# Kernel tuning notes

Hardware: AMD Instinct MI355X
Metric: run time of the kernel (lower is better)

Reference implementation:

```python
import jax, jax.numpy as jnp
import numpy as np

N, E, D = 100000, 1600000, 128


def setup_inputs() -> dict:
    key = jax.random.key(0)
    ks = jax.random.split(key, 8)
    s = 1.0 / np.sqrt(D)
    return {
        "x": jax.random.normal(ks[0], (N, D), dtype=jnp.float32),
        "edge_index": jax.random.randint(ks[1], (2, E), 0, N, dtype=jnp.int64),
        "x_prev": jax.random.normal(ks[2], (N, D), dtype=jnp.float32),
        # GCNConv params: weight [in,out], bias [out]
        "W": jax.random.uniform(ks[3], (D, D), jnp.float32, -s, s),
        "b": jnp.zeros((D,), jnp.float32),
        # GRUCell params (torch layout): [3*H, H] gates ordered (r, z, n)
        "W_ih": jax.random.uniform(ks[4], (3 * D, D), jnp.float32, -s, s),
        "W_hh": jax.random.uniform(ks[5], (3 * D, D), jnp.float32, -s, s),
        "b_ih": jax.random.uniform(ks[6], (3 * D,), jnp.float32, -s, s),
        "b_hh": jax.random.uniform(ks[7], (3 * D,), jnp.float32, -s, s),
    }


def _gcn_conv(x, edge_index, W, b):
    n = x.shape[0]
    loop = jnp.arange(n, dtype=edge_index.dtype)
    src = jnp.concatenate([edge_index[0], loop])  # [E+N]
    dst = jnp.concatenate([edge_index[1], loop])
    # symmetric normalization: deg over destinations (incl. self loops)
    deg = jax.ops.segment_sum(jnp.ones_like(dst, dtype=x.dtype), dst, num_segments=n)
    dinv = jnp.where(deg > 0, jax.lax.rsqrt(deg), 0.0)
    norm = dinv[src] * dinv[dst]  # [E+N]
    xw = x @ W  # [N, out]
    msg = xw[src] * norm[:, None]  # gather + scale
    return jax.ops.segment_sum(msg, dst, num_segments=n) + b


def _gru_cell(inp, h, W_ih, W_hh, b_ih, b_hh):
    gi = inp @ W_ih.T + b_ih  # [N, 3H]
    gh = h @ W_hh.T + b_hh
    i_r, i_z, i_n = jnp.split(gi, 3, axis=-1)
    h_r, h_z, h_n = jnp.split(gh, 3, axis=-1)
    r = jax.nn.sigmoid(i_r + h_r)
    z = jax.nn.sigmoid(i_z + h_z)
    ntil = jnp.tanh(i_n + r * h_n)
    return (1.0 - z) * ntil + z * h


def reference(x, edge_index, x_prev, W, b, W_ih, W_hh, b_ih, b_hh):
    h_cur = _gcn_conv(x, edge_index, W, b)
    return _gru_cell(h_cur, x_prev, W_ih, W_hh, b_ih, b_hh)
```

## Files before the change

kernel.cpp:

```cpp
#include <hip/hip_runtime.h>
#include <hip/hip_bf16.h>
#include <math.h>

#define DIM 128
#define PSHIFT 10
#define PSZ 1024
#define CHUNK 2048

typedef __attribute__((ext_vector_type(8))) short bf16x8;
typedef __attribute__((ext_vector_type(4))) float f32x4;
typedef unsigned short u16;
typedef unsigned int u32;
typedef unsigned long long u64;

__device__ __forceinline__ u16 f2bf(float x) {
    u32 u = __builtin_bit_cast(u32, x);
    u += 0x7fff + ((u >> 16) & 1);
    return (u16)(u >> 16);
}
__device__ __forceinline__ float bf2f(u16 h) {
    return __builtin_bit_cast(float, (u32)h << 16);
}


__global__ __launch_bounds__(256) void k_zero(int* __restrict__ p, int n) {
    int i = blockIdx.x * 256 + threadIdx.x;
    if (i < n) p[i] = 0;
}

__global__ __launch_bounds__(256) void k_pcount(const int* __restrict__ edst,
                                                int* __restrict__ pcnt, int E) {
    __shared__ int h[128];
    int t = threadIdx.x;
    if (t < 128) h[t] = 0;
    __syncthreads();
    int stride = gridDim.x * 256;
    for (int e = blockIdx.x * 256 + t; e < E; e += stride)
        atomicAdd(&h[edst[e] >> PSHIFT], 1);
    __syncthreads();
    if (t < 128 && h[t]) atomicAdd(&pcnt[t], h[t]);
}

__global__ __launch_bounds__(256) void k_pscan(const int* __restrict__ pcnt,
                                               int* __restrict__ poff,
                                               int* __restrict__ pfill,
                                               int* __restrict__ rowp,
                                               int P, int N, int E) {
    __shared__ int a[256];
    int t = threadIdx.x;
    int v = (t < P) ? pcnt[t] : 0;
    a[t] = v;
    __syncthreads();
    #pragma unroll
    for (int off = 1; off < 256; off <<= 1) {
        int y = (t >= off) ? a[t - off] : 0;
        __syncthreads();
        a[t] += y;
        __syncthreads();
    }
    int excl = a[t] - v;
    if (t < P) { poff[t] = excl; pfill[t] = excl; }
    if (t == 0) { poff[P] = E; rowp[N] = E; }
}

__global__ __launch_bounds__(256) void k_pscatter(const int* __restrict__ esrc,
                                                  const int* __restrict__ edst,
                                                  int* __restrict__ pfill,
                                                  u64* __restrict__ pbuf, int E) {
    __shared__ int hist[128], sc[128], lofs[128], gbase[128];
    __shared__ u32 ss[CHUNK], sd[CHUNK];
    int t = threadIdx.x;
    int c0 = blockIdx.x * CHUNK;
    int cnt = E - c0; if (cnt > CHUNK) cnt = CHUNK;

    if (t < 128) hist[t] = 0;
    __syncthreads();

    u32 s[8], d[8];
    int p[8], r[8];
    #pragma unroll
    for (int j = 0; j < 8; ++j) {
        int i = j * 256 + t;
        if (i < cnt) {
            s[j] = (u32)esrc[c0 + i];
            d[j] = (u32)edst[c0 + i];
            p[j] = (int)(d[j] >> PSHIFT);
            r[j] = atomicAdd(&hist[p[j]], 1);
        }
    }
    __syncthreads();

    if (t < 128) sc[t] = hist[t];
    __syncthreads();
    #pragma unroll
    for (int off = 1; off < 128; off <<= 1) {
        int y = 0;
        if (t < 128 && t >= off) y = sc[t - off];
        __syncthreads();
        if (t < 128) sc[t] += y;
        __syncthreads();
    }
    if (t < 128) {
        lofs[t] = sc[t] - hist[t];
        if (hist[t] > 0) gbase[t] = atomicAdd(&pfill[t], hist[t]);
    }
    __syncthreads();

    #pragma unroll
    for (int j = 0; j < 8; ++j) {
        int i = j * 256 + t;
        if (i < cnt) {
            int idx = lofs[p[j]] + r[j];
            ss[idx] = s[j];
            sd[idx] = d[j];
        }
    }
    __syncthreads();

    for (int i = t; i < cnt; i += 256) {
        u32 dd = sd[i];
        int pp = (int)(dd >> PSHIFT);
        int gpos = gbase[pp] + (i - lofs[pp]);
        pbuf[gpos] = (u64)ss[i] | ((u64)dd << 32);
    }
}

__global__ __launch_bounds__(256) void k_pfill(const u64* __restrict__ pbuf,
                                               const int* __restrict__ poff,
                                               int* __restrict__ rowp,
                                               int* __restrict__ srcs,
                                               float* __restrict__ dinv, int N) {
    __shared__ int cnt[PSZ];
    __shared__ int wsum[4];
    int p = blockIdx.x, t = threadIdx.x;
    int lane = t & 63, wid = t >> 6;
    int nb0 = p << PSHIFT;
    int ncnt = N - nb0; if (ncnt > PSZ) ncnt = PSZ;
    int b0 = poff[p], b1 = poff[p + 1];
    int bc = b1 - b0;

    for (int i = t; i < PSZ; i += 256) cnt[i] = 0;
    __syncthreads();
    for (int i = t; i < bc; i += 256) {
        u32 d = (u32)(pbuf[b0 + i] >> 32);
        atomicAdd(&cnt[d - nb0], 1);
    }
    __syncthreads();

    int base = t * 4;
    int c[4];
    int ssum = 0;
    #pragma unroll
    for (int j = 0; j < 4; ++j) { c[j] = cnt[base + j]; ssum += c[j]; }
    int incl = ssum;
    #pragma unroll
    for (int off = 1; off < 64; off <<= 1) {
        int y = __shfl_up(incl, off, 64);
        if (lane >= off) incl += y;
    }
    if (lane == 63) wsum[wid] = incl;
    __syncthreads();
    int add = 0;
    for (int w = 0; w < wid; ++w) add += wsum[w];
    int rr = b0 + add + (incl - ssum);
    #pragma unroll
    for (int j = 0; j < 4; ++j) {
        int i = base + j;
        if (i < ncnt) {
            rowp[nb0 + i] = rr;
            dinv[nb0 + i] = rsqrtf((float)(c[j] + 1));
        }
        cnt[i] = rr;
        rr += c[j];
    }
    __syncthreads();

    for (int i = t; i < bc; i += 256) {
        u64 v = pbuf[b0 + i];
        u32 sv = (u32)v;
        u32 d = (u32)(v >> 32);
        int pos = atomicAdd(&cnt[d - nb0], 1);
        srcs[pos] = (int)sv;
    }
}


__global__ __launch_bounds__(256) void k_prepw(const float* __restrict__ W,
                                               const float* __restrict__ Wih,
                                               const float* __restrict__ Whh,
                                               u16* __restrict__ Wt,
                                               u16* __restrict__ Wihb,
                                               u16* __restrict__ Whhb) {
    int i = blockIdx.x * 256 + threadIdx.x;
    if (i < 128 * 128) {
        int k = i >> 7, c = i & 127;
        Wt[c * 128 + k] = f2bf(W[i]);
    }
    if (i < 3 * 128 * 128) {
        Wihb[i] = f2bf(Wih[i]);
        Whhb[i] = f2bf(Whh[i]);
    }
}

__global__ __launch_bounds__(256) void k_cast1(const float4* __restrict__ a,
                                               u32* __restrict__ ab, int n4) {
    int stride = gridDim.x * 256;
    for (int i = blockIdx.x * 256 + threadIdx.x; i < n4; i += stride) {
        float4 v = a[i];
        ab[i * 2 + 0] = (u32)f2bf(v.x) | ((u32)f2bf(v.y) << 16);
        ab[i * 2 + 1] = (u32)f2bf(v.z) | ((u32)f2bf(v.w) << 16);
    }
}


__global__ __launch_bounds__(256) void k_gemm1(const float* __restrict__ X,
                                               const u16* __restrict__ Wt,
                                               u16* __restrict__ XWb, int n) {
    __shared__ u16 Wlds[128 * 128];
    int t = threadIdx.x, w = t >> 6, l = t & 63;
    int lr = l & 15, q = l >> 4;

    for (int cidx = t; cidx < 2048; cidx += 256) {
        int r = cidx >> 4, kc = cidx & 15;
        int dst = r * 128 + ((kc * 8) ^ ((r & 7) << 3));
        *(bf16x8*)(Wlds + dst) = *(const bf16x8*)(Wt + r * 128 + kc * 8);
    }
    __syncthreads();

    int r0 = blockIdx.x * 128;
    int wrow0 = r0 + w * 32;
    int sw = (lr & 7) << 3;
    int ar0 = wrow0 + lr;      if (ar0 > n - 1) ar0 = n - 1;
    int ar1 = wrow0 + 16 + lr; if (ar1 > n - 1) ar1 = n - 1;
    const float* x0 = X + (size_t)ar0 * DIM;
    const float* x1 = X + (size_t)ar1 * DIM;

    f32x4 acc[2][8];
    #pragma unroll
    for (int s = 0; s < 2; ++s)
        #pragma unroll
        for (int c = 0; c < 8; ++c) acc[s][c] = (f32x4){0.f, 0.f, 0.f, 0.f};

    #pragma unroll
    for (int kb = 0; kb < 4; ++kb) {
        int ko = kb * 32 + q * 8;
        float4 f00 = *(const float4*)(x0 + ko), f01 = *(const float4*)(x0 + ko + 4);
        float4 f10 = *(const float4*)(x1 + ko), f11 = *(const float4*)(x1 + ko + 4);
        bf16x8 a0, a1;
        a0[0] = (short)f2bf(f00.x); a0[1] = (short)f2bf(f00.y);
        a0[2] = (short)f2bf(f00.z); a0[3] = (short)f2bf(f00.w);
        a0[4] = (short)f2bf(f01.x); a0[5] = (short)f2bf(f01.y);
        a0[6] = (short)f2bf(f01.z); a0[7] = (short)f2bf(f01.w);
        a1[0] = (short)f2bf(f10.x); a1[1] = (short)f2bf(f10.y);
        a1[2] = (short)f2bf(f10.z); a1[3] = (short)f2bf(f10.w);
        a1[4] = (short)f2bf(f11.x); a1[5] = (short)f2bf(f11.y);
        a1[6] = (short)f2bf(f11.z); a1[7] = (short)f2bf(f11.w);
        int kw = ko ^ sw;
        #pragma unroll
        for (int ct = 0; ct < 8; ++ct) {
            bf16x8 b = *(const bf16x8*)(Wlds + (ct * 16 + lr) * 128 + kw);
            acc[0][ct] = __builtin_amdgcn_mfma_f32_16x16x32_bf16(a0, b, acc[0][ct], 0, 0, 0);
            acc[1][ct] = __builtin_amdgcn_mfma_f32_16x16x32_bf16(a1, b, acc[1][ct], 0, 0, 0);
        }
    }

    #pragma unroll
    for (int s = 0; s < 2; ++s)
        #pragma unroll
        for (int ct = 0; ct < 8; ++ct)
            #pragma unroll
            for (int i = 0; i < 4; ++i) {
                int row = wrow0 + s * 16 + q * 4 + i;
                if (row < n)
                    XWb[(size_t)row * DIM + ct * 16 + lr] = f2bf(acc[s][ct][i]);
            }
}


__global__ __launch_bounds__(256) void k_gather(const u16* __restrict__ XWb,
                                                const float* __restrict__ dinv,
                                                const int* __restrict__ row_ptr,
                                                const int* __restrict__ srcs,
                                                const float* __restrict__ bias,
                                                u16* __restrict__ Hcb, int n) {
    int node = blockIdx.x * 4 + (threadIdx.x >> 6);
    if (node >= n) return;
    int lane = threadIdx.x & 63;
    int c = lane * 2;

    float di = dinv[node];
    u32 sv = *(const u32*)(XWb + (size_t)node * DIM + c);
    float accx = bias[c]     + bf2f((u16)(sv & 0xffff)) * di * di;
    float accy = bias[c + 1] + bf2f((u16)(sv >> 16))    * di * di;

    int e = row_ptr[node], end = row_ptr[node + 1];
    for (; e + 3 < end; e += 4) {
        int s0 = srcs[e], s1 = srcs[e + 1], s2 = srcs[e + 2], s3 = srcs[e + 3];
        float n0 = dinv[s0] * di, n1 = dinv[s1] * di, n2 = dinv[s2] * di, n3 = dinv[s3] * di;
        u32 v0 = *(const u32*)(XWb + (size_t)s0 * DIM + c);
        u32 v1 = *(const u32*)(XWb + (size_t)s1 * DIM + c);
        u32 v2 = *(const u32*)(XWb + (size_t)s2 * DIM + c);
        u32 v3 = *(const u32*)(XWb + (size_t)s3 * DIM + c);
        accx += bf2f((u16)(v0 & 0xffff)) * n0 + bf2f((u16)(v1 & 0xffff)) * n1
              + bf2f((u16)(v2 & 0xffff)) * n2 + bf2f((u16)(v3 & 0xffff)) * n3;
        accy += bf2f((u16)(v0 >> 16)) * n0 + bf2f((u16)(v1 >> 16)) * n1
              + bf2f((u16)(v2 >> 16)) * n2 + bf2f((u16)(v3 >> 16)) * n3;
    }
    for (; e < end; ++e) {
        int s = srcs[e];
        float nrm = dinv[s] * di;
        u32 v = *(const u32*)(XWb + (size_t)s * DIM + c);
        accx += bf2f((u16)(v & 0xffff)) * nrm;
        accy += bf2f((u16)(v >> 16)) * nrm;
    }
    *(u32*)(Hcb + (size_t)node * DIM + c) = (u32)f2bf(accx) | ((u32)f2bf(accy) << 16);
}


__global__ __launch_bounds__(256) void k_gru(const u16* __restrict__ Hcb,
                                             const u16* __restrict__ Xpb,
                                             const u16* __restrict__ Wihb,
                                             const u16* __restrict__ Whhb,
                                             const float* __restrict__ bih,
                                             const float* __restrict__ bhh,
                                             float* __restrict__ Out, int n) {
    __shared__ u16 Wlds[96 * 128];
    int t = threadIdx.x, w = t >> 6, l = t & 63;
    int lr = l & 15, q = l >> 4;

    int nwg = gridDim.x;
    int qq = nwg >> 3, rr8 = nwg & 7;
    int xcd = blockIdx.x & 7, idx = blockIdx.x >> 3;
    int logical = (xcd < rr8 ? xcd * (qq + 1) : rr8 * (qq + 1) + (xcd - rr8) * qq) + idx;
    int cs = logical & 7;
    int rb = logical >> 3;
    int c0 = cs * 16;
    int r0 = rb * 128;

    for (int cidx = t; cidx < 1536; cidx += 256) {
        int r = cidx >> 4, kc = cidx & 15;
        int m = (r >= 48);
        int rr = m ? r - 48 : r;
        int g = rr >> 4, cc = rr & 15;
        const u16* src = (m ? Whhb : Wihb) + (size_t)((g << 7) + c0 + cc) * DIM + kc * 8;
        int dst = r * 128 + ((kc * 8) ^ ((r & 7) << 3));
        *(bf16x8*)(Wlds + dst) = *(const bf16x8*)src;
    }
    __syncthreads();

    int wrow0 = r0 + w * 32;
    int sw = (lr & 7) << 3;
    int ar0 = wrow0 + lr;      if (ar0 > n - 1) ar0 = n - 1;
    int ar1 = wrow0 + 16 + lr; if (ar1 > n - 1) ar1 = n - 1;
    const u16* hb0 = Hcb + (size_t)ar0 * DIM;
    const u16* hb1 = Hcb + (size_t)ar1 * DIM;
    const u16* xb0 = Xpb + (size_t)ar0 * DIM;
    const u16* xb1 = Xpb + (size_t)ar1 * DIM;

    f32x4 aI[3][2], aH[3][2];
    #pragma unroll
    for (int g = 0; g < 3; ++g)
        #pragma unroll
        for (int s = 0; s < 2; ++s) {
            aI[g][s] = (f32x4){0.f, 0.f, 0.f, 0.f};
            aH[g][s] = (f32x4){0.f, 0.f, 0.f, 0.f};
        }

    #pragma unroll
    for (int kb = 0; kb < 4; ++kb) {
        int ko = kb * 32 + q * 8;
        bf16x8 hA0 = *(const bf16x8*)(hb0 + ko);
        bf16x8 hA1 = *(const bf16x8*)(hb1 + ko);
        bf16x8 xA0 = *(const bf16x8*)(xb0 + ko);
        bf16x8 xA1 = *(const bf16x8*)(xb1 + ko);
        int kw = ko ^ sw;
        #pragma unroll
        for (int g = 0; g < 3; ++g) {
            int ridx = (g * 16 + lr) * 128 + kw;
            bf16x8 bI = *(const bf16x8*)(Wlds + ridx);
            bf16x8 bH = *(const bf16x8*)(Wlds + ridx + 48 * 128);
            aI[g][0] = __builtin_amdgcn_mfma_f32_16x16x32_bf16(hA0, bI, aI[g][0], 0, 0, 0);
            aI[g][1] = __builtin_amdgcn_mfma_f32_16x16x32_bf16(hA1, bI, aI[g][1], 0, 0, 0);
            aH[g][0] = __builtin_amdgcn_mfma_f32_16x16x32_bf16(xA0, bH, aH[g][0], 0, 0, 0);
            aH[g][1] = __builtin_amdgcn_mfma_f32_16x16x32_bf16(xA1, bH, aH[g][1], 0, 0, 0);
        }
    }

    int j = c0 + lr;
    float br = bih[j],       bz = bih[128 + j], bn = bih[256 + j];
    float cr = bhh[j],       cz = bhh[128 + j], cn = bhh[256 + j];
    #pragma unroll
    for (int s = 0; s < 2; ++s)
        #pragma unroll
        for (int i = 0; i < 4; ++i) {
            int row = wrow0 + s * 16 + q * 4 + i;
            if (row >= n) continue;
            float ir = aI[0][s][i] + br;
            float iz = aI[1][s][i] + bz;
            float in_ = aI[2][s][i] + bn;
            float hr = aH[0][s][i] + cr;
            float hz = aH[1][s][i] + cz;
            float hn = aH[2][s][i] + cn;
            float rg = 1.f / (1.f + __expf(-(ir + hr)));
            float zg = 1.f / (1.f + __expf(-(iz + hz)));
            float ng = tanhf(in_ + rg * hn);
            float hp = bf2f((u16)Xpb[(size_t)row * DIM + j]);
            Out[(size_t)row * DIM + j] = (1.f - zg) * ng + zg * hp;
        }
}


extern "C" void kernel_launch(void* const* d_in, const int* in_sizes, int n_in,
                              void* d_out, int out_size, void* d_ws, size_t ws_size,
                              hipStream_t stream) {
    const float* x     = (const float*)d_in[0];
    const int*   ei    = (const int*)d_in[1];
    const float* xprev = (const float*)d_in[2];
    const float* W     = (const float*)d_in[3];
    const float* b     = (const float*)d_in[4];
    const float* Wih   = (const float*)d_in[5];
    const float* Whh   = (const float*)d_in[6];
    const float* bih   = (const float*)d_in[7];
    const float* bhh   = (const float*)d_in[8];

    int N = in_sizes[0] / DIM;
    int E = in_sizes[1] / 2;
    int P = (N + PSZ - 1) >> PSHIFT;
    const int* esrc = ei;
    const int* edst = ei + E;

    char* p = (char*)d_ws;
    auto alloc = [&](size_t bytes) {
        char* q = p;
        p += (bytes + 255) & ~(size_t)255;
        return q;
    };
    float* dinv = (float*)alloc((size_t)N * 4);
    int*   rowp = (int*)  alloc((size_t)(N + 1) * 4);
    int*   srcs = (int*)  alloc((size_t)E * 4);
    u16*   Hcb  = (u16*)  alloc((size_t)N * DIM * 2);
    u16*   Xpb  = (u16*)  alloc((size_t)N * DIM * 2);
    u16*   XWb  = (u16*)  alloc((size_t)N * DIM * 2);
    u16*   Wt   = (u16*)  alloc(128 * 128 * 2);
    u16*   Wihb = (u16*)  alloc(3 * 128 * 128 * 2);
    u16*   Whhb = (u16*)  alloc(3 * 128 * 128 * 2);
    int*   pcnt = (int*)  alloc(128 * 4);
    int*   poff = (int*)  alloc(129 * 4);
    int*   pfil = (int*)  alloc(128 * 4);
    u64*   pbuf = (u64*)XWb;
    float* out  = (float*)d_out;

    k_zero    <<<1, 256, 0, stream>>>(pcnt, 128);
    k_pcount  <<<1024, 256, 0, stream>>>(edst, pcnt, E);
    k_pscan   <<<1, 256, 0, stream>>>(pcnt, poff, pfil, rowp, P, N, E);
    int nch = (E + CHUNK - 1) / CHUNK;
    k_pscatter<<<nch, 256, 0, stream>>>(esrc, edst, pfil, pbuf, E);
    k_pfill   <<<P, 256, 0, stream>>>(pbuf, poff, rowp, srcs, dinv, N);
    k_prepw   <<<192, 256, 0, stream>>>(W, Wih, Whh, Wt, Wihb, Whhb);
    int n4 = N * DIM / 4;
    k_cast1   <<<2048, 256, 0, stream>>>((const float4*)xprev, (u32*)Xpb, n4);
    int nrb = (N + 127) / 128;
    k_gemm1   <<<nrb, 256, 0, stream>>>(x, Wt, XWb, N);
    k_gather  <<<(N + 3) / 4, 256, 0, stream>>>(XWb, dinv, rowp, srcs, b, Hcb, N);
    k_gru     <<<nrb * 8, 256, 0, stream>>>(Hcb, Xpb, Wihb, Whhb, bih, bhh, out, N);
}
```

Before: 287.3 us.

## Persist GRU blocks, merge prep kernels, widen gather unroll, use fast activations

The GRU kernel becomes persistent: 1536 blocks loop over row blocks, so each block stages its weight slice into LDS once and reuses it across many row blocks. The weight-prep and x_prev cast kernels are merged into one launch. The gather loop now issues 8 independent edge loads per iteration instead of 4 to expose more memory-level parallelism. Sigmoid and tanh use hardware reciprocal and exp approximations. Costs are more register pressure in the gather and slightly lower activation accuracy.

```diff
diff --git a/kernel.cpp b/kernel.cpp
--- a/kernel.cpp
+++ b/kernel.cpp
@@ -20,6 +20,12 @@
 }
 __device__ __forceinline__ float bf2f(u16 h) {
     return __builtin_bit_cast(float, (u32)h << 16);
+}
+__device__ __forceinline__ float fsig(float x) {
+    return __builtin_amdgcn_rcpf(1.f + __expf(-x));
+}
+__device__ __forceinline__ float ftanh(float x) {
+    return 1.f - 2.f * __builtin_amdgcn_rcpf(__expf(2.f * x) + 1.f);
 }
 
 
@@ -185,30 +191,28 @@
 }
 
 
-__global__ __launch_bounds__(256) void k_prepw(const float* __restrict__ W,
-                                               const float* __restrict__ Wih,
-                                               const float* __restrict__ Whh,
-                                               u16* __restrict__ Wt,
-                                               u16* __restrict__ Wihb,
-                                               u16* __restrict__ Whhb) {
-    int i = blockIdx.x * 256 + threadIdx.x;
-    if (i < 128 * 128) {
-        int k = i >> 7, c = i & 127;
-        Wt[c * 128 + k] = f2bf(W[i]);
-    }
-    if (i < 3 * 128 * 128) {
-        Wihb[i] = f2bf(Wih[i]);
-        Whhb[i] = f2bf(Whh[i]);
-    }
-}
-
-__global__ __launch_bounds__(256) void k_cast1(const float4* __restrict__ a,
-                                               u32* __restrict__ ab, int n4) {
+__global__ __launch_bounds__(256) void k_prep(const float* __restrict__ W,
+                                              const float* __restrict__ Wih,
+                                              const float* __restrict__ Whh,
+                                              const float4* __restrict__ xp,
+                                              u16* __restrict__ Wt,
+                                              u16* __restrict__ Wihb,
+                                              u16* __restrict__ Whhb,
+                                              u32* __restrict__ Xpb, int n4) {
+    int gid = blockIdx.x * 256 + threadIdx.x;
     int stride = gridDim.x * 256;
-    for (int i = blockIdx.x * 256 + threadIdx.x; i < n4; i += stride) {
-        float4 v = a[i];
-        ab[i * 2 + 0] = (u32)f2bf(v.x) | ((u32)f2bf(v.y) << 16);
-        ab[i * 2 + 1] = (u32)f2bf(v.z) | ((u32)f2bf(v.w) << 16);
+    for (int i = gid; i < n4; i += stride) {
+        float4 v = xp[i];
+        Xpb[i * 2 + 0] = (u32)f2bf(v.x) | ((u32)f2bf(v.y) << 16);
+        Xpb[i * 2 + 1] = (u32)f2bf(v.z) | ((u32)f2bf(v.w) << 16);
+    }
+    if (gid < 128 * 128) {
+        int k = gid >> 7, c = gid & 127;
+        Wt[c * 128 + k] = f2bf(W[gid]);
+    }
+    if (gid < 3 * 128 * 128) {
+        Wihb[gid] = f2bf(Wih[gid]);
+        Whhb[gid] = f2bf(Whh[gid]);
     }
 }
 
@@ -294,17 +298,20 @@
     float accy = bias[c + 1] + bf2f((u16)(sv >> 16))    * di * di;
 
     int e = row_ptr[node], end = row_ptr[node + 1];
-    for (; e + 3 < end; e += 4) {
-        int s0 = srcs[e], s1 = srcs[e + 1], s2 = srcs[e + 2], s3 = srcs[e + 3];
-        float n0 = dinv[s0] * di, n1 = dinv[s1] * di, n2 = dinv[s2] * di, n3 = dinv[s3] * di;
-        u32 v0 = *(const u32*)(XWb + (size_t)s0 * DIM + c);
-        u32 v1 = *(const u32*)(XWb + (size_t)s1 * DIM + c);
-        u32 v2 = *(const u32*)(XWb + (size_t)s2 * DIM + c);
-        u32 v3 = *(const u32*)(XWb + (size_t)s3 * DIM + c);
-        accx += bf2f((u16)(v0 & 0xffff)) * n0 + bf2f((u16)(v1 & 0xffff)) * n1
-              + bf2f((u16)(v2 & 0xffff)) * n2 + bf2f((u16)(v3 & 0xffff)) * n3;
-        accy += bf2f((u16)(v0 >> 16)) * n0 + bf2f((u16)(v1 >> 16)) * n1
-              + bf2f((u16)(v2 >> 16)) * n2 + bf2f((u16)(v3 >> 16)) * n3;
+    for (; e + 7 < end; e += 8) {
+        int sdx[8]; float nw[8]; u32 vv[8];
+        #pragma unroll
+        for (int j = 0; j < 8; ++j) sdx[j] = srcs[e + j];
+        #pragma unroll
+        for (int j = 0; j < 8; ++j) nw[j] = dinv[sdx[j]] * di;
+        #pragma unroll
+        for (int j = 0; j < 8; ++j)
+            vv[j] = *(const u32*)(XWb + (size_t)sdx[j] * DIM + c);
+        #pragma unroll
+        for (int j = 0; j < 8; ++j) {
+            accx += bf2f((u16)(vv[j] & 0xffff)) * nw[j];
+            accy += bf2f((u16)(vv[j] >> 16)) * nw[j];
+        }
     }
     for (; e < end; ++e) {
         int s = srcs[e];
@@ -333,9 +340,9 @@
     int xcd = blockIdx.x & 7, idx = blockIdx.x >> 3;
     int logical = (xcd < rr8 ? xcd * (qq + 1) : rr8 * (qq + 1) + (xcd - rr8) * qq) + idx;
     int cs = logical & 7;
-    int rb = logical >> 3;
+    int slot = logical >> 3;
+    int nslot = nwg >> 3;
     int c0 = cs * 16;
-    int r0 = rb * 128;
 
     for (int cidx = t; cidx < 1536; cidx += 256) {
         int r = cidx >> 4, kc = cidx & 15;
@@ -348,65 +355,69 @@
     }
     __syncthreads();
 
-    int wrow0 = r0 + w * 32;
     int sw = (lr & 7) << 3;
-    int ar0 = wrow0 + lr;      if (ar0 > n - 1) ar0 = n - 1;
-    int ar1 = wrow0 + 16 + lr; if (ar1 > n - 1) ar1 = n - 1;
-    const u16* hb0 = Hcb + (size_t)ar0 * DIM;
-    const u16* hb1 = Hcb + (size_t)ar1 * DIM;
-    const u16* xb0 = Xpb + (size_t)ar0 * DIM;
-    const u16* xb1 = Xpb + (size_t)ar1 * DIM;
-
-    f32x4 aI[3][2], aH[3][2];
-    #pragma unroll
-    for (int g = 0; g < 3; ++g)
-        #pragma unroll
-        for (int s = 0; s < 2; ++s) {
-            aI[g][s] = (f32x4){0.f, 0.f, 0.f, 0.f};
-            aH[g][s] = (f32x4){0.f, 0.f, 0.f, 0.f};
-        }
-
-    #pragma unroll
-    for (int kb = 0; kb < 4; ++kb) {
-        int ko = kb * 32 + q * 8;
-        bf16x8 hA0 = *(const bf16x8*)(hb0 + ko);
-        bf16x8 hA1 = *(const bf16x8*)(hb1 + ko);
-        bf16x8 xA0 = *(const bf16x8*)(xb0 + ko);
-        bf16x8 xA1 = *(const bf16x8*)(xb1 + ko);
-        int kw = ko ^ sw;
-        #pragma unroll
-        for (int g = 0; g < 3; ++g) {
-            int ridx = (g * 16 + lr) * 128 + kw;
-            bf16x8 bI = *(const bf16x8*)(Wlds + ridx);
-            bf16x8 bH = *(const bf16x8*)(Wlds + ridx + 48 * 128);
-            aI[g][0] = __builtin_amdgcn_mfma_f32_16x16x32_bf16(hA0, bI, aI[g][0], 0, 0, 0);
-            aI[g][1] = __builtin_amdgcn_mfma_f32_16x16x32_bf16(hA1, bI, aI[g][1], 0, 0, 0);
-            aH[g][0] = __builtin_amdgcn_mfma_f32_16x16x32_bf16(xA0, bH, aH[g][0], 0, 0, 0);
-            aH[g][1] = __builtin_amdgcn_mfma_f32_16x16x32_bf16(xA1, bH, aH[g][1], 0, 0, 0);
-        }
-    }
-
     int j = c0 + lr;
     float br = bih[j],       bz = bih[128 + j], bn = bih[256 + j];
     float cr = bhh[j],       cz = bhh[128 + j], cn = bhh[256 + j];
-    #pragma unroll
-    for (int s = 0; s < 2; ++s)
-        #pragma unroll
-        for (int i = 0; i < 4; ++i) {
-            int row = wrow0 + s * 16 + q * 4 + i;
-            if (row >= n) continue;
-            float ir = aI[0][s][i] + br;
-            float iz = aI[1][s][i] + bz;
-            float in_ = aI[2][s][i] + bn;
-            float hr = aH[0][s][i] + cr;
-            float hz = aH[1][s][i] + cz;
-            float hn = aH[2][s][i] + cn;
-            float rg = 1.f / (1.f + __expf(-(ir + hr)));
-            float zg = 1.f / (1.f + __expf(-(iz + hz)));
-            float ng = tanhf(in_ + rg * hn);
-            float hp = bf2f((u16)Xpb[(size_t)row * DIM + j]);
-            Out[(size_t)row * DIM + j] = (1.f - zg) * ng + zg * hp;
-        }
+
+    int nrb = (n + 127) >> 7;
+    for (int rb = slot; rb < nrb; rb += nslot) {
+        int wrow0 = rb * 128 + w * 32;
+        int ar0 = wrow0 + lr;      if (ar0 > n - 1) ar0 = n - 1;
+        int ar1 = wrow0 + 16 + lr; if (ar1 > n - 1) ar1 = n - 1;
+        const u16* hb0 = Hcb + (size_t)ar0 * DIM;
+        const u16* hb1 = Hcb + (size_t)ar1 * DIM;
+        const u16* xb0 = Xpb + (size_t)ar0 * DIM;
+        const u16* xb1 = Xpb + (size_t)ar1 * DIM;
+
+        f32x4 aI[3][2], aH[3][2];
+        #pragma unroll
+        for (int g = 0; g < 3; ++g)
+            #pragma unroll
+            for (int s = 0; s < 2; ++s) {
+                aI[g][s] = (f32x4){0.f, 0.f, 0.f, 0.f};
+                aH[g][s] = (f32x4){0.f, 0.f, 0.f, 0.f};
+            }
+
+        #pragma unroll
+        for (int kb = 0; kb < 4; ++kb) {
+            int ko = kb * 32 + q * 8;
+            bf16x8 hA0 = *(const bf16x8*)(hb0 + ko);
+            bf16x8 hA1 = *(const bf16x8*)(hb1 + ko);
+            bf16x8 xA0 = *(const bf16x8*)(xb0 + ko);
+            bf16x8 xA1 = *(const bf16x8*)(xb1 + ko);
+            int kw = ko ^ sw;
+            #pragma unroll
+            for (int g = 0; g < 3; ++g) {
+                int ridx = (g * 16 + lr) * 128 + kw;
+                bf16x8 bI = *(const bf16x8*)(Wlds + ridx);
+                bf16x8 bH = *(const bf16x8*)(Wlds + ridx + 48 * 128);
+                aI[g][0] = __builtin_amdgcn_mfma_f32_16x16x32_bf16(hA0, bI, aI[g][0], 0, 0, 0);
+                aI[g][1] = __builtin_amdgcn_mfma_f32_16x16x32_bf16(hA1, bI, aI[g][1], 0, 0, 0);
+                aH[g][0] = __builtin_amdgcn_mfma_f32_16x16x32_bf16(xA0, bH, aH[g][0], 0, 0, 0);
+                aH[g][1] = __builtin_amdgcn_mfma_f32_16x16x32_bf16(xA1, bH, aH[g][1], 0, 0, 0);
+            }
+        }
+
+        #pragma unroll
+        for (int s = 0; s < 2; ++s)
+            #pragma unroll
+            for (int i = 0; i < 4; ++i) {
+                int row = wrow0 + s * 16 + q * 4 + i;
+                if (row >= n) continue;
+                float ir = aI[0][s][i] + br;
+                float iz = aI[1][s][i] + bz;
+                float in_ = aI[2][s][i] + bn;
+                float hr = aH[0][s][i] + cr;
+                float hz = aH[1][s][i] + cz;
+                float hn = aH[2][s][i] + cn;
+                float rg = fsig(ir + hr);
+                float zg = fsig(iz + hz);
+                float ng = ftanh(in_ + rg * hn);
+                float hp = bf2f((u16)Xpb[(size_t)row * DIM + j]);
+                Out[(size_t)row * DIM + j] = (1.f - zg) * ng + zg * hp;
+            }
+    }
 }
 
 
@@ -456,11 +467,11 @@
     int nch = (E + CHUNK - 1) / CHUNK;
     k_pscatter<<<nch, 256, 0, stream>>>(esrc, edst, pfil, pbuf, E);
     k_pfill   <<<P, 256, 0, stream>>>(pbuf, poff, rowp, srcs, dinv, N);
-    k_prepw   <<<192, 256, 0, stream>>>(W, Wih, Whh, Wt, Wihb, Whhb);
     int n4 = N * DIM / 4;
-    k_cast1   <<<2048, 256, 0, stream>>>((const float4*)xprev, (u32*)Xpb, n4);
+    k_prep    <<<2048, 256, 0, stream>>>(W, Wih, Whh, (const float4*)xprev,
+                                         Wt, Wihb, Whhb, (u32*)Xpb, n4);
     int nrb = (N + 127) / 128;
     k_gemm1   <<<nrb, 256, 0, stream>>>(x, Wt, XWb, N);
     k_gather  <<<(N + 3) / 4, 256, 0, stream>>>(XWb, dinv, rowp, srcs, b, Hcb, N);
-    k_gru     <<<nrb * 8, 256, 0, stream>>>(Hcb, Xpb, Wihb, Whhb, bih, bhh, out, N);
-}
+    k_gru     <<<1536, 256, 0, stream>>>(Hcb, Xpb, Wihb, Whhb, bih, bhh, out, N);
+}
```

New measurement: 279.9 us. 2.6% less time.
